# Performance work log

Measured on AMD Instinct MI355X. Metric: run time of the kernel, lower is better.

Reference implementation:

```python
import jax, jax.numpy as jnp
import numpy as np

TEMPERATURE = 0.07  # init kwarg 'temperature'


def setup_inputs() -> dict:
    key = jax.random.key(0)
    k1, k2, k3 = jax.random.split(key, 3)
    N, E = 8192, 128
    return {
        "audio_embeds": jax.random.normal(k1, (N, E), dtype=jnp.float32),
        "text_embeds": jax.random.normal(k2, (N, E), dtype=jnp.float32),
        "fids": jax.random.randint(k3, (N,), 0, 4096),
    }


def reference(audio_embeds, text_embeds, fids):
    # Per-sample loop in the original is equivalent to a full NxN score matrix
    # with a symmetric fid-equality mask (diagonal always kept):
    #   row i valid set  = {j : fid[j] != fid[i]} U {i}
    # L_it(i) = CE over S[i, valid] with target i  (A_i vs sampled texts)
    # L_ai(i) = CE over S[valid, i] with target i  (sampled audios vs T_i)
    S = jnp.matmul(audio_embeds, text_embeds.T) / TEMPERATURE  # [N, N], S[j, i] = <A_j, T_i>/t
    N = S.shape[0]
    mask = (fids[:, None] != fids[None, :]) | jnp.eye(N, dtype=bool)  # symmetric
    neg = jnp.finfo(S.dtype).min
    Sm = jnp.where(mask, S, neg)
    diag = jnp.diagonal(S)
    L_it = jax.nn.logsumexp(Sm, axis=1) - diag  # row-wise CE at diagonal target
    L_ai = jax.nn.logsumexp(Sm, axis=0) - diag  # column-wise CE at diagonal target
    return jnp.mean(L_ai + L_it)
```

## Files before the change

kernel.cpp:

```cpp
#include <hip/hip_runtime.h>
#include <hip/hip_bf16.h>
#include <math.h>

#define NN 8192
#define EE 128

static constexpr float INV_T = 1.0f / 0.07f;
static constexpr float LOG2E = 1.4426950408889634f;
static constexpr float LN2   = 0.6931471805599453f;
static constexpr float SENT  = -3.0e38f;

typedef __attribute__((ext_vector_type(8))) short fragAB;
typedef __attribute__((ext_vector_type(4))) float f32x4;
typedef const __attribute__((address_space(1))) void gvoid;
typedef __attribute__((address_space(3))) void lvoid;

__device__ inline float fexp2(float x) { float r; asm("v_exp_f32 %0, %1" : "=v"(r) : "v"(x)); return r; }
__device__ inline float flog2(float x) { float r; asm("v_log_f32 %0, %1" : "=v"(r) : "v"(x)); return r; }

template<int CTRL>
__device__ inline float dpp_f(float x) {
  return __builtin_bit_cast(float,
      __builtin_amdgcn_update_dpp(0, __builtin_bit_cast(int, x), CTRL, 0xf, 0xf, true));
}
__device__ inline float red16_max(float x) {
  x = fmaxf(x, dpp_f<0xB1>(x));
  x = fmaxf(x, dpp_f<0x4E>(x));
  x = fmaxf(x, dpp_f<0x141>(x));
  x = fmaxf(x, dpp_f<0x140>(x));
  return x;
}
__device__ inline float red16_add(float x) {
  x += dpp_f<0xB1>(x); x += dpp_f<0x4E>(x); x += dpp_f<0x141>(x); x += dpp_f<0x140>(x);
  return x;
}

__device__ inline ushort f32_to_bf16_bits(float x) {
  union { float f; unsigned u; } c; c.f = x;
  unsigned u = c.u;
  u += 0x7fffu + ((u >> 16) & 1u);
  return (ushort)(u >> 16);
}

__global__ void lsl_cvt_kernel(const float* __restrict__ A, const float* __restrict__ T,
                               ushort* __restrict__ Ab, ushort* __restrict__ Tb,
                               float* __restrict__ diag) {
  const int t = blockIdx.x * 256 + threadIdx.x;
  const int i = t * 4;
  float4 a = *reinterpret_cast<const float4*>(A + i);
  float4 tt = *reinterpret_cast<const float4*>(T + i);
  ushort4 oa, ot;
  const float SC = INV_T * LOG2E;
  oa.x = f32_to_bf16_bits(a.x * SC); oa.y = f32_to_bf16_bits(a.y * SC);
  oa.z = f32_to_bf16_bits(a.z * SC); oa.w = f32_to_bf16_bits(a.w * SC);
  ot.x = f32_to_bf16_bits(tt.x); ot.y = f32_to_bf16_bits(tt.y);
  ot.z = f32_to_bf16_bits(tt.z); ot.w = f32_to_bf16_bits(tt.w);
  *reinterpret_cast<ushort4*>(Ab + i) = oa;
  *reinterpret_cast<ushort4*>(Tb + i) = ot;

  float pd = a.x * tt.x + a.y * tt.y + a.z * tt.z + a.w * tt.w;
  pd += __shfl_xor(pd, 1); pd += __shfl_xor(pd, 2); pd += __shfl_xor(pd, 4);
  pd += __shfl_xor(pd, 8); pd += __shfl_xor(pd, 16);
  if ((threadIdx.x & 31) == 0) diag[i >> 7] = pd * (INV_T * LOG2E);
}

__global__ __launch_bounds__(512, 4) void
lsl_tile_kernel(const ushort* __restrict__ Ab, const ushort* __restrict__ Tb,
                const int* __restrict__ fids,
                float2* __restrict__ rowp, float2* __restrict__ colp) {
  __shared__ ushort As[128 * 128];
  __shared__ ushort Bs[128 * 128];
  __shared__ float2 cscr[4 * 64];

  const int bid = blockIdx.x;
  const int swz = (bid & 7) * 512 + (bid >> 3);
  const int tm = swz >> 6, tn = swz & 63;
  const int tid = threadIdx.x;
  const int lane = tid & 63;
  const int wid  = tid >> 6;
  const int wm = wid >> 1;
  const int wn = wid & 1;
  const int rbase = tm * 128 + wm * 32;
  const int cbase = tn * 128 + wn * 64;
  const int lr = lane & 15, lg = lane >> 4;

  {
    const int trow = tid >> 4;
    const int scol = ((tid & 15) ^ (trow & 15)) * 8;
    const ushort* gA = Ab + (size_t)(tm * 128 + trow) * EE + scol;
    const ushort* gB = Tb + (size_t)(tn * 128 + trow) * EE + scol;
#pragma unroll
    for (int i = 0; i < 4; ++i)
      __builtin_amdgcn_global_load_lds((gvoid*)(gA + (size_t)i * 32 * EE),
          (lvoid*)((char*)As + i * 8192 + wid * 1024), 16, 0, 0);
#pragma unroll
    for (int i = 0; i < 4; ++i)
      __builtin_amdgcn_global_load_lds((gvoid*)(gB + (size_t)i * 32 * EE),
          (lvoid*)((char*)Bs + i * 8192 + wid * 1024), 16, 0, 0);
  }
  __syncthreads();

  f32x4 acc[2][4] = {};
#pragma unroll
  for (int ks = 0; ks < 4; ++ks) {
    fragAB av[2], bv[4];
#pragma unroll
    for (int f = 0; f < 2; ++f)
      av[f] = *reinterpret_cast<const fragAB*>(
          &As[(wm * 32 + f * 16 + lr) * 128 + (((ks * 4 + lg) ^ lr) * 8)]);
#pragma unroll
    for (int f = 0; f < 4; ++f)
      bv[f] = *reinterpret_cast<const fragAB*>(
          &Bs[(wn * 64 + f * 16 + lr) * 128 + (((ks * 4 + lg) ^ lr) * 8)]);
#pragma unroll
    for (int fm = 0; fm < 2; ++fm)
#pragma unroll
      for (int fn = 0; fn < 4; ++fn)
        acc[fm][fn] = __builtin_amdgcn_mfma_f32_16x16x32_bf16(av[fm], bv[fn], acc[fm][fn], 0, 0, 0);
  }

  int fr[2][4], fc[4];
#pragma unroll
  for (int fm = 0; fm < 2; ++fm) {
    int4 v4 = *reinterpret_cast<const int4*>(fids + rbase + fm * 16 + lg * 4);
    fr[fm][0] = v4.x; fr[fm][1] = v4.y; fr[fm][2] = v4.z; fr[fm][3] = v4.w;
  }
#pragma unroll
  for (int fn = 0; fn < 4; ++fn) fc[fn] = fids[cbase + fn * 16 + lr];

  float e[2][4][4];
  const bool dt = (tm == tn) && ((wm >> 1) == wn);
  const int dfb = (wm & 1) * 2;
#pragma unroll
  for (int fm = 0; fm < 2; ++fm)
#pragma unroll
    for (int fn = 0; fn < 4; ++fn)
#pragma unroll
      for (int r = 0; r < 4; ++r) {
        float v = acc[fm][fn][r];
        bool keep = (fr[fm][r] != fc[fn]) || (dt && fn == dfb + fm && lr == lg * 4 + r);
        e[fm][fn][r] = keep ? v : SENT;
      }

  float rm[2][4];
#pragma unroll
  for (int fm = 0; fm < 2; ++fm)
#pragma unroll
    for (int r = 0; r < 4; ++r)
      rm[fm][r] = fmaxf(fmaxf(e[fm][0][r], e[fm][1][r]),
                        fmaxf(e[fm][2][r], e[fm][3][r]));
#pragma unroll
  for (int fm = 0; fm < 2; ++fm)
#pragma unroll
    for (int r = 0; r < 4; ++r)
      rm[fm][r] = red16_max(rm[fm][r]);

  float rs[2][4];
#pragma unroll
  for (int fm = 0; fm < 2; ++fm)
#pragma unroll
    for (int r = 0; r < 4; ++r)
      rs[fm][r] = (fexp2(e[fm][0][r] - rm[fm][r]) + fexp2(e[fm][1][r] - rm[fm][r]))
                + (fexp2(e[fm][2][r] - rm[fm][r]) + fexp2(e[fm][3][r] - rm[fm][r]));
#pragma unroll
  for (int fm = 0; fm < 2; ++fm)
#pragma unroll
    for (int r = 0; r < 4; ++r)
      rs[fm][r] = red16_add(rs[fm][r]);

  const int rblk = tn * 2 + wn;
  if (lr == 0) {
#pragma unroll
    for (int fm = 0; fm < 2; ++fm)
#pragma unroll
      for (int r = 0; r < 4; ++r)
        rowp[(size_t)rblk * NN + (rbase + fm * 16 + lg * 4 + r)] = make_float2(rm[fm][r], rs[fm][r]);
  }

  float cm[4];
#pragma unroll
  for (int fn = 0; fn < 4; ++fn) {
    float m0 = fmaxf(fmaxf(e[0][fn][0], e[0][fn][1]), fmaxf(e[0][fn][2], e[0][fn][3]));
    float m1 = fmaxf(fmaxf(e[1][fn][0], e[1][fn][1]), fmaxf(e[1][fn][2], e[1][fn][3]));
    cm[fn] = fmaxf(m0, m1);
  }
  {
    float t0 = __shfl_xor(cm[0], 16), t1 = __shfl_xor(cm[1], 16),
          t2 = __shfl_xor(cm[2], 16), t3 = __shfl_xor(cm[3], 16);
    cm[0] = fmaxf(cm[0], t0); cm[1] = fmaxf(cm[1], t1);
    cm[2] = fmaxf(cm[2], t2); cm[3] = fmaxf(cm[3], t3);
    t0 = __shfl_xor(cm[0], 32); t1 = __shfl_xor(cm[1], 32);
    t2 = __shfl_xor(cm[2], 32); t3 = __shfl_xor(cm[3], 32);
    cm[0] = fmaxf(cm[0], t0); cm[1] = fmaxf(cm[1], t1);
    cm[2] = fmaxf(cm[2], t2); cm[3] = fmaxf(cm[3], t3);
  }
  float cs[4];
#pragma unroll
  for (int fn = 0; fn < 4; ++fn) {
    float s0 = (fexp2(e[0][fn][0] - cm[fn]) + fexp2(e[0][fn][1] - cm[fn]))
             + (fexp2(e[0][fn][2] - cm[fn]) + fexp2(e[0][fn][3] - cm[fn]));
    float s1 = (fexp2(e[1][fn][0] - cm[fn]) + fexp2(e[1][fn][1] - cm[fn]))
             + (fexp2(e[1][fn][2] - cm[fn]) + fexp2(e[1][fn][3] - cm[fn]));
    cs[fn] = s0 + s1;
  }
  {
    float t0 = __shfl_xor(cs[0], 16), t1 = __shfl_xor(cs[1], 16),
          t2 = __shfl_xor(cs[2], 16), t3 = __shfl_xor(cs[3], 16);
    cs[0] += t0; cs[1] += t1; cs[2] += t2; cs[3] += t3;
    t0 = __shfl_xor(cs[0], 32); t1 = __shfl_xor(cs[1], 32);
    t2 = __shfl_xor(cs[2], 32); t3 = __shfl_xor(cs[3], 32);
    cs[0] += t0; cs[1] += t1; cs[2] += t2; cs[3] += t3;
  }

  const int pi = (wm >> 1) * 2 + wn;
  if ((wm & 1) == 1 && lg == 0) {
#pragma unroll
    for (int fn = 0; fn < 4; ++fn)
      cscr[pi * 64 + fn * 16 + lr] = make_float2(cm[fn], cs[fn]);
  }
  __syncthreads();
  if ((wm & 1) == 0 && lg == 0) {
    const int cblk = tm * 2 + (wm >> 1);
#pragma unroll
    for (int fn = 0; fn < 4; ++fn) {
      float2 o = cscr[pi * 64 + fn * 16 + lr];
      float M = fmaxf(cm[fn], o.x);
      float S = cs[fn] * fexp2(cm[fn] - M) + o.y * fexp2(o.x - M);
      colp[(size_t)cblk * NN + (cbase + fn * 16 + lr)] = make_float2(M, S);
    }
  }
}

__global__ __launch_bounds__(256) void
lsl_merge_kernel(const float2* __restrict__ rowp, const float2* __restrict__ colp,
                 const float* __restrict__ diag, float* __restrict__ bsum) {
  __shared__ float2 sl[128 * 33];
  __shared__ float2 red[32][8];
  const int tid = threadIdx.x;
  const int ibase = blockIdx.x * 32;
  const int s = tid & 31, p = tid >> 5;

  float lse0 = 0.f, lse1 = 0.f;
#pragma unroll
  for (int pass = 0; pass < 2; ++pass) {
    const float2* __restrict__ src = pass ? colp : rowp;
#pragma unroll
    for (int k = 0; k < 16; ++k) {
      int L = tid + k * 256;
      int b = L >> 5, di = L & 31;
      sl[b * 33 + di] = src[(size_t)b * NN + ibase + di];
    }
    __syncthreads();
    float m = SENT;
#pragma unroll
    for (int k = 0; k < 16; ++k) m = fmaxf(m, sl[(p * 16 + k) * 33 + s].x);
    float sum = 0.f;
#pragma unroll
    for (int k = 0; k < 16; ++k) {
      float2 v = sl[(p * 16 + k) * 33 + s];
      sum += v.y * fexp2(v.x - m);
    }
    red[s][p] = make_float2(m, sum);
    __syncthreads();
    if (p == 0) {
      float M = SENT;
#pragma unroll
      for (int k = 0; k < 8; ++k) M = fmaxf(M, red[s][k].x);
      float S = 0.f;
#pragma unroll
      for (int k = 0; k < 8; ++k) S += red[s][k].y * fexp2(red[s][k].x - M);
      if (pass == 0) lse0 = M + flog2(S); else lse1 = M + flog2(S);
    }
    __syncthreads();
  }

  if (tid < 32) {
    float loss = lse0 + lse1 - 2.f * diag[ibase + tid];
#pragma unroll
    for (int d = 1; d < 32; d <<= 1) loss += __shfl_xor(loss, d);
    if (tid == 0) bsum[blockIdx.x] = loss;
  }
}

__global__ __launch_bounds__(256) void
lsl_final_kernel(const float* __restrict__ bsum, float* __restrict__ out) {
  float v = bsum[threadIdx.x];
#pragma unroll
  for (int d = 1; d < 64; d <<= 1) v += __shfl_xor(v, d);
  __shared__ float l4[4];
  if ((threadIdx.x & 63) == 0) l4[threadIdx.x >> 6] = v;
  __syncthreads();
  if (threadIdx.x == 0) out[0] = (l4[0] + l4[1] + l4[2] + l4[3]) * (LN2 / (float)NN);
}

extern "C" void kernel_launch(void* const* d_in, const int* in_sizes, int n_in,
                              void* d_out, int out_size, void* d_ws, size_t ws_size,
                              hipStream_t stream) {
  const float* A = (const float*)d_in[0];
  const float* T = (const float*)d_in[1];
  const int* fids = (const int*)d_in[2];
  float* out = (float*)d_out;
  char* ws = (char*)d_ws;

  size_t off = 0;
  ushort* Ab  = (ushort*)(ws + off); off += (size_t)NN * EE * 2;
  ushort* Tb  = (ushort*)(ws + off); off += (size_t)NN * EE * 2;
  float* diag = (float*)(ws + off);  off += (size_t)NN * 4;
  float2* rowp = (float2*)(ws + off); off += (size_t)NN * 128 * 8;
  float2* colp = (float2*)(ws + off); off += (size_t)NN * 128 * 8;
  float* bsum = (float*)(ws + off);  off += 1024;

  hipLaunchKernelGGL(lsl_cvt_kernel, dim3(NN * EE / 4 / 256), dim3(256), 0, stream, A, T, Ab, Tb, diag);
  hipLaunchKernelGGL(lsl_tile_kernel, dim3(4096), dim3(512), 0, stream, Ab, Tb, fids, rowp, colp);
  hipLaunchKernelGGL(lsl_merge_kernel, dim3(NN / 32), dim3(256), 0, stream, rowp, colp, diag, bsum);
  hipLaunchKernelGGL(lsl_final_kernel, dim3(1), dim3(256), 0, stream, bsum, out);
}
```

Baseline: 63.65 us.

## Process two column tiles per block, prefetching second B tile during epilogue

Each block now handles two adjacent 128-column tiles, keeping the A tile resident in LDS and halving the grid. The second B tile is loaded asynchronously into LDS while the first tile's masked logsumexp epilogue runs, overlapping memory traffic with the exp/reduction work. This removes reloading of A and hides some load latency. The cost is fewer blocks for latency hiding, longer per-block serial work, and an extra barrier.

```diff
diff --git a/kernel.cpp b/kernel.cpp
--- a/kernel.cpp
+++ b/kernel.cpp
@@ -73,22 +73,22 @@
   __shared__ float2 cscr[4 * 64];
 
   const int bid = blockIdx.x;
-  const int swz = (bid & 7) * 512 + (bid >> 3);
-  const int tm = swz >> 6, tn = swz & 63;
+  const int swz = (bid & 7) * 256 + (bid >> 3);
+  const int tm = swz >> 5, tnp = swz & 31;
   const int tid = threadIdx.x;
   const int lane = tid & 63;
   const int wid  = tid >> 6;
   const int wm = wid >> 1;
   const int wn = wid & 1;
   const int rbase = tm * 128 + wm * 32;
-  const int cbase = tn * 128 + wn * 64;
   const int lr = lane & 15, lg = lane >> 4;
 
+  const int trow = tid >> 4;
+  const int scol = ((tid & 15) ^ (trow & 15)) * 8;
+
   {
-    const int trow = tid >> 4;
-    const int scol = ((tid & 15) ^ (trow & 15)) * 8;
     const ushort* gA = Ab + (size_t)(tm * 128 + trow) * EE + scol;
-    const ushort* gB = Tb + (size_t)(tn * 128 + trow) * EE + scol;
+    const ushort* gB = Tb + (size_t)(tnp * 256 + trow) * EE + scol;
 #pragma unroll
     for (int i = 0; i < 4; ++i)
       __builtin_amdgcn_global_load_lds((gvoid*)(gA + (size_t)i * 32 * EE),
@@ -98,6 +98,123 @@
       __builtin_amdgcn_global_load_lds((gvoid*)(gB + (size_t)i * 32 * EE),
           (lvoid*)((char*)Bs + i * 8192 + wid * 1024), 16, 0, 0);
   }
+
+  int fr[2][4];
+#pragma unroll
+  for (int fm = 0; fm < 2; ++fm) {
+    int4 v4 = *reinterpret_cast<const int4*>(fids + rbase + fm * 16 + lg * 4);
+    fr[fm][0] = v4.x; fr[fm][1] = v4.y; fr[fm][2] = v4.z; fr[fm][3] = v4.w;
+  }
+
+  auto epilogue = [&](f32x4 (&acc)[2][4], int tn) {
+    const int cbase = tn * 128 + wn * 64;
+    int fc[4];
+#pragma unroll
+    for (int fn = 0; fn < 4; ++fn) fc[fn] = fids[cbase + fn * 16 + lr];
+
+    float e[2][4][4];
+    const bool dt = (tm == tn) && ((wm >> 1) == wn);
+    const int dfb = (wm & 1) * 2;
+#pragma unroll
+    for (int fm = 0; fm < 2; ++fm)
+#pragma unroll
+      for (int fn = 0; fn < 4; ++fn)
+#pragma unroll
+        for (int r = 0; r < 4; ++r) {
+          float v = acc[fm][fn][r];
+          bool keep = (fr[fm][r] != fc[fn]) || (dt && fn == dfb + fm && lr == lg * 4 + r);
+          e[fm][fn][r] = keep ? v : SENT;
+        }
+
+    float rm[2][4];
+#pragma unroll
+    for (int fm = 0; fm < 2; ++fm)
+#pragma unroll
+      for (int r = 0; r < 4; ++r)
+        rm[fm][r] = fmaxf(fmaxf(e[fm][0][r], e[fm][1][r]),
+                          fmaxf(e[fm][2][r], e[fm][3][r]));
+#pragma unroll
+    for (int fm = 0; fm < 2; ++fm)
+#pragma unroll
+      for (int r = 0; r < 4; ++r)
+        rm[fm][r] = red16_max(rm[fm][r]);
+
+    float rs[2][4];
+#pragma unroll
+    for (int fm = 0; fm < 2; ++fm)
+#pragma unroll
+      for (int r = 0; r < 4; ++r)
+        rs[fm][r] = (fexp2(e[fm][0][r] - rm[fm][r]) + fexp2(e[fm][1][r] - rm[fm][r]))
+                  + (fexp2(e[fm][2][r] - rm[fm][r]) + fexp2(e[fm][3][r] - rm[fm][r]));
+#pragma unroll
+    for (int fm = 0; fm < 2; ++fm)
+#pragma unroll
+      for (int r = 0; r < 4; ++r)
+        rs[fm][r] = red16_add(rs[fm][r]);
+
+    const int rblk = tn * 2 + wn;
+    if (lr == 0) {
+#pragma unroll
+      for (int fm = 0; fm < 2; ++fm)
+#pragma unroll
+        for (int r = 0; r < 4; ++r)
+          rowp[(size_t)rblk * NN + (rbase + fm * 16 + lg * 4 + r)] = make_float2(rm[fm][r], rs[fm][r]);
+    }
+
+    float cm[4];
+#pragma unroll
+    for (int fn = 0; fn < 4; ++fn) {
+      float m0 = fmaxf(fmaxf(e[0][fn][0], e[0][fn][1]), fmaxf(e[0][fn][2], e[0][fn][3]));
+      float m1 = fmaxf(fmaxf(e[1][fn][0], e[1][fn][1]), fmaxf(e[1][fn][2], e[1][fn][3]));
+      cm[fn] = fmaxf(m0, m1);
+    }
+    {
+      float t0 = __shfl_xor(cm[0], 16), t1 = __shfl_xor(cm[1], 16),
+            t2 = __shfl_xor(cm[2], 16), t3 = __shfl_xor(cm[3], 16);
+      cm[0] = fmaxf(cm[0], t0); cm[1] = fmaxf(cm[1], t1);
+      cm[2] = fmaxf(cm[2], t2); cm[3] = fmaxf(cm[3], t3);
+      t0 = __shfl_xor(cm[0], 32); t1 = __shfl_xor(cm[1], 32);
+      t2 = __shfl_xor(cm[2], 32); t3 = __shfl_xor(cm[3], 32);
+      cm[0] = fmaxf(cm[0], t0); cm[1] = fmaxf(cm[1], t1);
+      cm[2] = fmaxf(cm[2], t2); cm[3] = fmaxf(cm[3], t3);
+    }
+    float cs[4];
+#pragma unroll
+    for (int fn = 0; fn < 4; ++fn) {
+      float s0 = (fexp2(e[0][fn][0] - cm[fn]) + fexp2(e[0][fn][1] - cm[fn]))
+               + (fexp2(e[0][fn][2] - cm[fn]) + fexp2(e[0][fn][3] - cm[fn]));
+      float s1 = (fexp2(e[1][fn][0] - cm[fn]) + fexp2(e[1][fn][1] - cm[fn]))
+               + (fexp2(e[1][fn][2] - cm[fn]) + fexp2(e[1][fn][3] - cm[fn]));
+      cs[fn] = s0 + s1;
+    }
+    {
+      float t0 = __shfl_xor(cs[0], 16), t1 = __shfl_xor(cs[1], 16),
+            t2 = __shfl_xor(cs[2], 16), t3 = __shfl_xor(cs[3], 16);
+      cs[0] += t0; cs[1] += t1; cs[2] += t2; cs[3] += t3;
+      t0 = __shfl_xor(cs[0], 32); t1 = __shfl_xor(cs[1], 32);
+      t2 = __shfl_xor(cs[2], 32); t3 = __shfl_xor(cs[3], 32);
+      cs[0] += t0; cs[1] += t1; cs[2] += t2; cs[3] += t3;
+    }
+
+    const int pi = (wm >> 1) * 2 + wn;
+    if ((wm & 1) == 1 && lg == 0) {
+#pragma unroll
+      for (int fn = 0; fn < 4; ++fn)
+        cscr[pi * 64 + fn * 16 + lr] = make_float2(cm[fn], cs[fn]);
+    }
+    __syncthreads();
+    if ((wm & 1) == 0 && lg == 0) {
+      const int cblk = tm * 2 + (wm >> 1);
+#pragma unroll
+      for (int fn = 0; fn < 4; ++fn) {
+        float2 o = cscr[pi * 64 + fn * 16 + lr];
+        float M = fmaxf(cm[fn], o.x);
+        float S = cs[fn] * fexp2(cm[fn] - M) + o.y * fexp2(o.x - M);
+        colp[(size_t)cblk * NN + (cbase + fn * 16 + lr)] = make_float2(M, S);
+      }
+    }
+  };
+
   __syncthreads();
 
   f32x4 acc[2][4] = {};
@@ -119,116 +236,40 @@
         acc[fm][fn] = __builtin_amdgcn_mfma_f32_16x16x32_bf16(av[fm], bv[fn], acc[fm][fn], 0, 0, 0);
   }
 
-  int fr[2][4], fc[4];
-#pragma unroll
-  for (int fm = 0; fm < 2; ++fm) {
-    int4 v4 = *reinterpret_cast<const int4*>(fids + rbase + fm * 16 + lg * 4);
-    fr[fm][0] = v4.x; fr[fm][1] = v4.y; fr[fm][2] = v4.z; fr[fm][3] = v4.w;
-  }
-#pragma unroll
-  for (int fn = 0; fn < 4; ++fn) fc[fn] = fids[cbase + fn * 16 + lr];
-
-  float e[2][4][4];
-  const bool dt = (tm == tn) && ((wm >> 1) == wn);
-  const int dfb = (wm & 1) * 2;
-#pragma unroll
-  for (int fm = 0; fm < 2; ++fm)
-#pragma unroll
-    for (int fn = 0; fn < 4; ++fn)
-#pragma unroll
-      for (int r = 0; r < 4; ++r) {
-        float v = acc[fm][fn][r];
-        bool keep = (fr[fm][r] != fc[fn]) || (dt && fn == dfb + fm && lr == lg * 4 + r);
-        e[fm][fn][r] = keep ? v : SENT;
-      }
-
-  float rm[2][4];
-#pragma unroll
-  for (int fm = 0; fm < 2; ++fm)
-#pragma unroll
-    for (int r = 0; r < 4; ++r)
-      rm[fm][r] = fmaxf(fmaxf(e[fm][0][r], e[fm][1][r]),
-                        fmaxf(e[fm][2][r], e[fm][3][r]));
-#pragma unroll
-  for (int fm = 0; fm < 2; ++fm)
-#pragma unroll
-    for (int r = 0; r < 4; ++r)
-      rm[fm][r] = red16_max(rm[fm][r]);
-
-  float rs[2][4];
-#pragma unroll
-  for (int fm = 0; fm < 2; ++fm)
-#pragma unroll
-    for (int r = 0; r < 4; ++r)
-      rs[fm][r] = (fexp2(e[fm][0][r] - rm[fm][r]) + fexp2(e[fm][1][r] - rm[fm][r]))
-                + (fexp2(e[fm][2][r] - rm[fm][r]) + fexp2(e[fm][3][r] - rm[fm][r]));
-#pragma unroll
-  for (int fm = 0; fm < 2; ++fm)
-#pragma unroll
-    for (int r = 0; r < 4; ++r)
-      rs[fm][r] = red16_add(rs[fm][r]);
-
-  const int rblk = tn * 2 + wn;
-  if (lr == 0) {
-#pragma unroll
-    for (int fm = 0; fm < 2; ++fm)
-#pragma unroll
-      for (int r = 0; r < 4; ++r)
-        rowp[(size_t)rblk * NN + (rbase + fm * 16 + lg * 4 + r)] = make_float2(rm[fm][r], rs[fm][r]);
-  }
-
-  float cm[4];
-#pragma unroll
-  for (int fn = 0; fn < 4; ++fn) {
-    float m0 = fmaxf(fmaxf(e[0][fn][0], e[0][fn][1]), fmaxf(e[0][fn][2], e[0][fn][3]));
-    float m1 = fmaxf(fmaxf(e[1][fn][0], e[1][fn][1]), fmaxf(e[1][fn][2], e[1][fn][3]));
-    cm[fn] = fmaxf(m0, m1);
-  }
+  __syncthreads();
+
   {
-    float t0 = __shfl_xor(cm[0], 16), t1 = __shfl_xor(cm[1], 16),
-          t2 = __shfl_xor(cm[2], 16), t3 = __shfl_xor(cm[3], 16);
-    cm[0] = fmaxf(cm[0], t0); cm[1] = fmaxf(cm[1], t1);
-    cm[2] = fmaxf(cm[2], t2); cm[3] = fmaxf(cm[3], t3);
-    t0 = __shfl_xor(cm[0], 32); t1 = __shfl_xor(cm[1], 32);
-    t2 = __shfl_xor(cm[2], 32); t3 = __shfl_xor(cm[3], 32);
-    cm[0] = fmaxf(cm[0], t0); cm[1] = fmaxf(cm[1], t1);
-    cm[2] = fmaxf(cm[2], t2); cm[3] = fmaxf(cm[3], t3);
-  }
-  float cs[4];
-#pragma unroll
-  for (int fn = 0; fn < 4; ++fn) {
-    float s0 = (fexp2(e[0][fn][0] - cm[fn]) + fexp2(e[0][fn][1] - cm[fn]))
-             + (fexp2(e[0][fn][2] - cm[fn]) + fexp2(e[0][fn][3] - cm[fn]));
-    float s1 = (fexp2(e[1][fn][0] - cm[fn]) + fexp2(e[1][fn][1] - cm[fn]))
-             + (fexp2(e[1][fn][2] - cm[fn]) + fexp2(e[1][fn][3] - cm[fn]));
-    cs[fn] = s0 + s1;
-  }
-  {
-    float t0 = __shfl_xor(cs[0], 16), t1 = __shfl_xor(cs[1], 16),
-          t2 = __shfl_xor(cs[2], 16), t3 = __shfl_xor(cs[3], 16);
-    cs[0] += t0; cs[1] += t1; cs[2] += t2; cs[3] += t3;
-    t0 = __shfl_xor(cs[0], 32); t1 = __shfl_xor(cs[1], 32);
-    t2 = __shfl_xor(cs[2], 32); t3 = __shfl_xor(cs[3], 32);
-    cs[0] += t0; cs[1] += t1; cs[2] += t2; cs[3] += t3;
-  }
-
-  const int pi = (wm >> 1) * 2 + wn;
-  if ((wm & 1) == 1 && lg == 0) {
-#pragma unroll
-    for (int fn = 0; fn < 4; ++fn)
-      cscr[pi * 64 + fn * 16 + lr] = make_float2(cm[fn], cs[fn]);
-  }
+    const ushort* gB2 = Tb + (size_t)(tnp * 256 + 128 + trow) * EE + scol;
+#pragma unroll
+    for (int i = 0; i < 4; ++i)
+      __builtin_amdgcn_global_load_lds((gvoid*)(gB2 + (size_t)i * 32 * EE),
+          (lvoid*)((char*)Bs + i * 8192 + wid * 1024), 16, 0, 0);
+  }
+
+  epilogue(acc, tnp * 2);
+
   __syncthreads();
-  if ((wm & 1) == 0 && lg == 0) {
-    const int cblk = tm * 2 + (wm >> 1);
-#pragma unroll
-    for (int fn = 0; fn < 4; ++fn) {
-      float2 o = cscr[pi * 64 + fn * 16 + lr];
-      float M = fmaxf(cm[fn], o.x);
-      float S = cs[fn] * fexp2(cm[fn] - M) + o.y * fexp2(o.x - M);
-      colp[(size_t)cblk * NN + (cbase + fn * 16 + lr)] = make_float2(M, S);
-    }
-  }
+
+  f32x4 acc2[2][4] = {};
+#pragma unroll
+  for (int ks = 0; ks < 4; ++ks) {
+    fragAB av[2], bv[4];
+#pragma unroll
+    for (int f = 0; f < 2; ++f)
+      av[f] = *reinterpret_cast<const fragAB*>(
+          &As[(wm * 32 + f * 16 + lr) * 128 + (((ks * 4 + lg) ^ lr) * 8)]);
+#pragma unroll
+    for (int f = 0; f < 4; ++f)
+      bv[f] = *reinterpret_cast<const fragAB*>(
+          &Bs[(wn * 64 + f * 16 + lr) * 128 + (((ks * 4 + lg) ^ lr) * 8)]);
+#pragma unroll
+    for (int fm = 0; fm < 2; ++fm)
+#pragma unroll
+      for (int fn = 0; fn < 4; ++fn)
+        acc2[fm][fn] = __builtin_amdgcn_mfma_f32_16x16x32_bf16(av[fm], bv[fn], acc2[fm][fn], 0, 0, 0);
+  }
+
+  epilogue(acc2, tnp * 2 + 1);
 }
 
 __global__ __launch_bounds__(256) void
@@ -311,7 +352,7 @@
   float* bsum = (float*)(ws + off);  off += 1024;
 
   hipLaunchKernelGGL(lsl_cvt_kernel, dim3(NN * EE / 4 / 256), dim3(256), 0, stream, A, T, Ab, Tb, diag);
-  hipLaunchKernelGGL(lsl_tile_kernel, dim3(4096), dim3(512), 0, stream, Ab, Tb, fids, rowp, colp);
+  hipLaunchKernelGGL(lsl_tile_kernel, dim3(2048), dim3(512), 0, stream, Ab, Tb, fids, rowp, colp);
   hipLaunchKernelGGL(lsl_merge_kernel, dim3(NN / 32), dim3(256), 0, stream, rowp, colp, diag, bsum);
   hipLaunchKernelGGL(lsl_final_kernel, dim3(1), dim3(256), 0, stream, bsum, out);
 }
```

Result: faster. 61.59 us (median of 2 runs) (-3.2%).

## Reuse A tile across four column sub-tiles and halve column partials

Applied to the files above, without the earlier changes.

Each tile block now keeps its 128-row A tile in LDS and walks 256 columns in four 64-column stages. The next B half-tile is loaded into a single shared buffer while the current stage's masked row/column reductions run, and the grid drops from 4096 to 2048 blocks. Column partials are merged across all eight waves inside the block, so the column-partial buffer and the merge kernel's column pass shrink from 128 to 64 partial blocks. The goal is less redundant A loading, smaller LDS use per block (allowing more resident blocks) and less partial traffic, at the cost of extra barriers per stage and a serial load-then-compute dependency on one B buffer.

```diff
diff --git a/kernel.cpp b/kernel.cpp
--- a/kernel.cpp
+++ b/kernel.cpp
@@ -64,169 +64,159 @@
   if ((threadIdx.x & 31) == 0) diag[i >> 7] = pd * (INV_T * LOG2E);
 }
 
-__global__ __launch_bounds__(512, 4) void
+__global__ __launch_bounds__(512, 6) void
 lsl_tile_kernel(const ushort* __restrict__ Ab, const ushort* __restrict__ Tb,
                 const int* __restrict__ fids,
                 float2* __restrict__ rowp, float2* __restrict__ colp) {
   __shared__ ushort As[128 * 128];
-  __shared__ ushort Bs[128 * 128];
-  __shared__ float2 cscr[4 * 64];
+  __shared__ ushort Bs[64 * 128];
+  __shared__ float2 cscr[8 * 64];
 
   const int bid = blockIdx.x;
-  const int swz = (bid & 7) * 512 + (bid >> 3);
-  const int tm = swz >> 6, tn = swz & 63;
+  const int swz = (bid & 7) * 256 + (bid >> 3);
+  const int tm = swz >> 5, tnq = swz & 31;
   const int tid = threadIdx.x;
   const int lane = tid & 63;
   const int wid  = tid >> 6;
-  const int wm = wid >> 1;
-  const int wn = wid & 1;
-  const int rbase = tm * 128 + wm * 32;
-  const int cbase = tn * 128 + wn * 64;
+  const int rbase = tm * 128 + wid * 16;
   const int lr = lane & 15, lg = lane >> 4;
 
+  const int trow = tid >> 4;
+  const int scol = ((tid & 15) ^ (trow & 15)) * 8;
+
+  auto stageB = [&](int tn, int h) {
+    const ushort* gB = Tb + (size_t)(tn * 128 + h * 64 + trow) * EE + scol;
+#pragma unroll
+    for (int i = 0; i < 2; ++i)
+      __builtin_amdgcn_global_load_lds((gvoid*)(gB + (size_t)i * 32 * EE),
+          (lvoid*)((char*)Bs + i * 8192 + wid * 1024), 16, 0, 0);
+  };
+
   {
-    const int trow = tid >> 4;
-    const int scol = ((tid & 15) ^ (trow & 15)) * 8;
     const ushort* gA = Ab + (size_t)(tm * 128 + trow) * EE + scol;
-    const ushort* gB = Tb + (size_t)(tn * 128 + trow) * EE + scol;
 #pragma unroll
     for (int i = 0; i < 4; ++i)
       __builtin_amdgcn_global_load_lds((gvoid*)(gA + (size_t)i * 32 * EE),
           (lvoid*)((char*)As + i * 8192 + wid * 1024), 16, 0, 0);
-#pragma unroll
-    for (int i = 0; i < 4; ++i)
-      __builtin_amdgcn_global_load_lds((gvoid*)(gB + (size_t)i * 32 * EE),
-          (lvoid*)((char*)Bs + i * 8192 + wid * 1024), 16, 0, 0);
-  }
+  }
+  stageB(tnq * 2, 0);
+
+  int fr[4];
+  {
+    int4 v4 = *reinterpret_cast<const int4*>(fids + rbase + lg * 4);
+    fr[0] = v4.x; fr[1] = v4.y; fr[2] = v4.z; fr[3] = v4.w;
+  }
+
   __syncthreads();
 
-  f32x4 acc[2][4] = {};
-#pragma unroll
-  for (int ks = 0; ks < 4; ++ks) {
-    fragAB av[2], bv[4];
-#pragma unroll
-    for (int f = 0; f < 2; ++f)
-      av[f] = *reinterpret_cast<const fragAB*>(
-          &As[(wm * 32 + f * 16 + lr) * 128 + (((ks * 4 + lg) ^ lr) * 8)]);
-#pragma unroll
-    for (int f = 0; f < 4; ++f)
-      bv[f] = *reinterpret_cast<const fragAB*>(
-          &Bs[(wn * 64 + f * 16 + lr) * 128 + (((ks * 4 + lg) ^ lr) * 8)]);
-#pragma unroll
-    for (int fm = 0; fm < 2; ++fm)
+#pragma unroll
+  for (int s = 0; s < 4; ++s) {
+    const int q = s >> 1, h = s & 1;
+    const int tn = tnq * 2 + q;
+    const int cbase = tn * 128 + h * 64;
+
+    f32x4 acc[4] = {};
+#pragma unroll
+    for (int ks = 0; ks < 4; ++ks) {
+      fragAB av, bv[4];
+      av = *reinterpret_cast<const fragAB*>(
+          &As[(wid * 16 + lr) * 128 + (((ks * 4 + lg) ^ lr) * 8)]);
+#pragma unroll
+      for (int f = 0; f < 4; ++f)
+        bv[f] = *reinterpret_cast<const fragAB*>(
+            &Bs[(f * 16 + lr) * 128 + (((ks * 4 + lg) ^ lr) * 8)]);
 #pragma unroll
       for (int fn = 0; fn < 4; ++fn)
-        acc[fm][fn] = __builtin_amdgcn_mfma_f32_16x16x32_bf16(av[fm], bv[fn], acc[fm][fn], 0, 0, 0);
-  }
-
-  int fr[2][4], fc[4];
-#pragma unroll
-  for (int fm = 0; fm < 2; ++fm) {
-    int4 v4 = *reinterpret_cast<const int4*>(fids + rbase + fm * 16 + lg * 4);
-    fr[fm][0] = v4.x; fr[fm][1] = v4.y; fr[fm][2] = v4.z; fr[fm][3] = v4.w;
-  }
-#pragma unroll
-  for (int fn = 0; fn < 4; ++fn) fc[fn] = fids[cbase + fn * 16 + lr];
-
-  float e[2][4][4];
-  const bool dt = (tm == tn) && ((wm >> 1) == wn);
-  const int dfb = (wm & 1) * 2;
-#pragma unroll
-  for (int fm = 0; fm < 2; ++fm)
+        acc[fn] = __builtin_amdgcn_mfma_f32_16x16x32_bf16(av, bv[fn], acc[fn], 0, 0, 0);
+    }
+
+    __syncthreads();
+
+    if (s < 3) stageB(tnq * 2 + ((s + 1) >> 1), (s + 1) & 1);
+
+    int fc[4];
+#pragma unroll
+    for (int fn = 0; fn < 4; ++fn) fc[fn] = fids[cbase + fn * 16 + lr];
+
+    float e[4][4];
+    const bool dt = (tm == tn) && ((wid >> 2) == h);
+    const int dfn = wid & 3;
 #pragma unroll
     for (int fn = 0; fn < 4; ++fn)
 #pragma unroll
       for (int r = 0; r < 4; ++r) {
-        float v = acc[fm][fn][r];
-        bool keep = (fr[fm][r] != fc[fn]) || (dt && fn == dfb + fm && lr == lg * 4 + r);
-        e[fm][fn][r] = keep ? v : SENT;
+        float v = acc[fn][r];
+        bool keep = (fr[r] != fc[fn]) || (dt && fn == dfn && lr == lg * 4 + r);
+        e[fn][r] = keep ? v : SENT;
       }
 
-  float rm[2][4];
-#pragma unroll
-  for (int fm = 0; fm < 2; ++fm)
+    float rm[4], rs[4];
 #pragma unroll
     for (int r = 0; r < 4; ++r)
-      rm[fm][r] = fmaxf(fmaxf(e[fm][0][r], e[fm][1][r]),
-                        fmaxf(e[fm][2][r], e[fm][3][r]));
-#pragma unroll
-  for (int fm = 0; fm < 2; ++fm)
+      rm[r] = fmaxf(fmaxf(e[0][r], e[1][r]), fmaxf(e[2][r], e[3][r]));
+#pragma unroll
+    for (int r = 0; r < 4; ++r) rm[r] = red16_max(rm[r]);
 #pragma unroll
     for (int r = 0; r < 4; ++r)
-      rm[fm][r] = red16_max(rm[fm][r]);
-
-  float rs[2][4];
-#pragma unroll
-  for (int fm = 0; fm < 2; ++fm)
-#pragma unroll
-    for (int r = 0; r < 4; ++r)
-      rs[fm][r] = (fexp2(e[fm][0][r] - rm[fm][r]) + fexp2(e[fm][1][r] - rm[fm][r]))
-                + (fexp2(e[fm][2][r] - rm[fm][r]) + fexp2(e[fm][3][r] - rm[fm][r]));
-#pragma unroll
-  for (int fm = 0; fm < 2; ++fm)
-#pragma unroll
-    for (int r = 0; r < 4; ++r)
-      rs[fm][r] = red16_add(rs[fm][r]);
-
-  const int rblk = tn * 2 + wn;
-  if (lr == 0) {
-#pragma unroll
-    for (int fm = 0; fm < 2; ++fm)
+      rs[r] = (fexp2(e[0][r] - rm[r]) + fexp2(e[1][r] - rm[r]))
+            + (fexp2(e[2][r] - rm[r]) + fexp2(e[3][r] - rm[r]));
+#pragma unroll
+    for (int r = 0; r < 4; ++r) rs[r] = red16_add(rs[r]);
+
+    const int rblk = tn * 2 + h;
+    if (lr == 0) {
 #pragma unroll
       for (int r = 0; r < 4; ++r)
-        rowp[(size_t)rblk * NN + (rbase + fm * 16 + lg * 4 + r)] = make_float2(rm[fm][r], rs[fm][r]);
-  }
-
-  float cm[4];
-#pragma unroll
-  for (int fn = 0; fn < 4; ++fn) {
-    float m0 = fmaxf(fmaxf(e[0][fn][0], e[0][fn][1]), fmaxf(e[0][fn][2], e[0][fn][3]));
-    float m1 = fmaxf(fmaxf(e[1][fn][0], e[1][fn][1]), fmaxf(e[1][fn][2], e[1][fn][3]));
-    cm[fn] = fmaxf(m0, m1);
-  }
-  {
-    float t0 = __shfl_xor(cm[0], 16), t1 = __shfl_xor(cm[1], 16),
-          t2 = __shfl_xor(cm[2], 16), t3 = __shfl_xor(cm[3], 16);
-    cm[0] = fmaxf(cm[0], t0); cm[1] = fmaxf(cm[1], t1);
-    cm[2] = fmaxf(cm[2], t2); cm[3] = fmaxf(cm[3], t3);
-    t0 = __shfl_xor(cm[0], 32); t1 = __shfl_xor(cm[1], 32);
-    t2 = __shfl_xor(cm[2], 32); t3 = __shfl_xor(cm[3], 32);
-    cm[0] = fmaxf(cm[0], t0); cm[1] = fmaxf(cm[1], t1);
-    cm[2] = fmaxf(cm[2], t2); cm[3] = fmaxf(cm[3], t3);
-  }
-  float cs[4];
-#pragma unroll
-  for (int fn = 0; fn < 4; ++fn) {
-    float s0 = (fexp2(e[0][fn][0] - cm[fn]) + fexp2(e[0][fn][1] - cm[fn]))
-             + (fexp2(e[0][fn][2] - cm[fn]) + fexp2(e[0][fn][3] - cm[fn]));
-    float s1 = (fexp2(e[1][fn][0] - cm[fn]) + fexp2(e[1][fn][1] - cm[fn]))
-             + (fexp2(e[1][fn][2] - cm[fn]) + fexp2(e[1][fn][3] - cm[fn]));
-    cs[fn] = s0 + s1;
-  }
-  {
-    float t0 = __shfl_xor(cs[0], 16), t1 = __shfl_xor(cs[1], 16),
-          t2 = __shfl_xor(cs[2], 16), t3 = __shfl_xor(cs[3], 16);
-    cs[0] += t0; cs[1] += t1; cs[2] += t2; cs[3] += t3;
-    t0 = __shfl_xor(cs[0], 32); t1 = __shfl_xor(cs[1], 32);
-    t2 = __shfl_xor(cs[2], 32); t3 = __shfl_xor(cs[3], 32);
-    cs[0] += t0; cs[1] += t1; cs[2] += t2; cs[3] += t3;
-  }
-
-  const int pi = (wm >> 1) * 2 + wn;
-  if ((wm & 1) == 1 && lg == 0) {
+        rowp[(size_t)rblk * NN + (rbase + lg * 4 + r)] = make_float2(rm[r], rs[r]);
+    }
+
+    float cm[4], cs[4];
 #pragma unroll
     for (int fn = 0; fn < 4; ++fn)
-      cscr[pi * 64 + fn * 16 + lr] = make_float2(cm[fn], cs[fn]);
-  }
-  __syncthreads();
-  if ((wm & 1) == 0 && lg == 0) {
-    const int cblk = tm * 2 + (wm >> 1);
-#pragma unroll
-    for (int fn = 0; fn < 4; ++fn) {
-      float2 o = cscr[pi * 64 + fn * 16 + lr];
-      float M = fmaxf(cm[fn], o.x);
-      float S = cs[fn] * fexp2(cm[fn] - M) + o.y * fexp2(o.x - M);
-      colp[(size_t)cblk * NN + (cbase + fn * 16 + lr)] = make_float2(M, S);
+      cm[fn] = fmaxf(fmaxf(e[fn][0], e[fn][1]), fmaxf(e[fn][2], e[fn][3]));
+    {
+      float t0 = __shfl_xor(cm[0], 16), t1 = __shfl_xor(cm[1], 16),
+            t2 = __shfl_xor(cm[2], 16), t3 = __shfl_xor(cm[3], 16);
+      cm[0] = fmaxf(cm[0], t0); cm[1] = fmaxf(cm[1], t1);
+      cm[2] = fmaxf(cm[2], t2); cm[3] = fmaxf(cm[3], t3);
+      t0 = __shfl_xor(cm[0], 32); t1 = __shfl_xor(cm[1], 32);
+      t2 = __shfl_xor(cm[2], 32); t3 = __shfl_xor(cm[3], 32);
+      cm[0] = fmaxf(cm[0], t0); cm[1] = fmaxf(cm[1], t1);
+      cm[2] = fmaxf(cm[2], t2); cm[3] = fmaxf(cm[3], t3);
+    }
+#pragma unroll
+    for (int fn = 0; fn < 4; ++fn)
+      cs[fn] = (fexp2(e[fn][0] - cm[fn]) + fexp2(e[fn][1] - cm[fn]))
+             + (fexp2(e[fn][2] - cm[fn]) + fexp2(e[fn][3] - cm[fn]));
+    {
+      float t0 = __shfl_xor(cs[0], 16), t1 = __shfl_xor(cs[1], 16),
+            t2 = __shfl_xor(cs[2], 16), t3 = __shfl_xor(cs[3], 16);
+      cs[0] += t0; cs[1] += t1; cs[2] += t2; cs[3] += t3;
+      t0 = __shfl_xor(cs[0], 32); t1 = __shfl_xor(cs[1], 32);
+      t2 = __shfl_xor(cs[2], 32); t3 = __shfl_xor(cs[3], 32);
+      cs[0] += t0; cs[1] += t1; cs[2] += t2; cs[3] += t3;
+    }
+
+    if (lg == 0) {
+#pragma unroll
+      for (int fn = 0; fn < 4; ++fn)
+        cscr[wid * 64 + fn * 16 + lr] = make_float2(cm[fn], cs[fn]);
+    }
+
+    __syncthreads();
+
+    if (lane < 8) {
+      const int c = wid * 8 + lane;
+      float M = cscr[c].x;
+#pragma unroll
+      for (int w = 1; w < 8; ++w) M = fmaxf(M, cscr[w * 64 + c].x);
+      float S = 0.f;
+#pragma unroll
+      for (int w = 0; w < 8; ++w) {
+        float2 p = cscr[w * 64 + c];
+        S += p.y * fexp2(p.x - M);
+      }
+      colp[(size_t)tm * NN + (cbase + c)] = make_float2(M, S);
     }
   }
 }
@@ -241,23 +231,21 @@
   const int s = tid & 31, p = tid >> 5;
 
   float lse0 = 0.f, lse1 = 0.f;
-#pragma unroll
   for (int pass = 0; pass < 2; ++pass) {
     const float2* __restrict__ src = pass ? colp : rowp;
-#pragma unroll
-    for (int k = 0; k < 16; ++k) {
+    const int NB = pass ? 64 : 128;
+    const int PB = NB >> 3;
+    for (int k = 0; k < (NB >> 3); ++k) {
       int L = tid + k * 256;
       int b = L >> 5, di = L & 31;
       sl[b * 33 + di] = src[(size_t)b * NN + ibase + di];
     }
     __syncthreads();
     float m = SENT;
-#pragma unroll
-    for (int k = 0; k < 16; ++k) m = fmaxf(m, sl[(p * 16 + k) * 33 + s].x);
+    for (int k = 0; k < PB; ++k) m = fmaxf(m, sl[(p * PB + k) * 33 + s].x);
     float sum = 0.f;
-#pragma unroll
-    for (int k = 0; k < 16; ++k) {
-      float2 v = sl[(p * 16 + k) * 33 + s];
+    for (int k = 0; k < PB; ++k) {
+      float2 v = sl[(p * PB + k) * 33 + s];
       sum += v.y * fexp2(v.x - m);
     }
     red[s][p] = make_float2(m, sum);
@@ -307,11 +295,11 @@
   ushort* Tb  = (ushort*)(ws + off); off += (size_t)NN * EE * 2;
   float* diag = (float*)(ws + off);  off += (size_t)NN * 4;
   float2* rowp = (float2*)(ws + off); off += (size_t)NN * 128 * 8;
-  float2* colp = (float2*)(ws + off); off += (size_t)NN * 128 * 8;
+  float2* colp = (float2*)(ws + off); off += (size_t)NN * 64 * 8;
   float* bsum = (float*)(ws + off);  off += 1024;
 
   hipLaunchKernelGGL(lsl_cvt_kernel, dim3(NN * EE / 4 / 256), dim3(256), 0, stream, A, T, Ab, Tb, diag);
-  hipLaunchKernelGGL(lsl_tile_kernel, dim3(4096), dim3(512), 0, stream, Ab, Tb, fids, rowp, colp);
+  hipLaunchKernelGGL(lsl_tile_kernel, dim3(2048), dim3(512), 0, stream, Ab, Tb, fids, rowp, colp);
   hipLaunchKernelGGL(lsl_merge_kernel, dim3(NN / 32), dim3(256), 0, stream, rowp, colp, diag, bsum);
   hipLaunchKernelGGL(lsl_final_kernel, dim3(1), dim3(256), 0, stream, bsum, out);
 }
```

After: 64.65 us. About the same (+1.6%).
